# Optimization experiments

Measured on AMD Instinct MI355X. Metric: run time of the kernel, lower is better.

## Reference

```python
import jax, jax.numpy as jnp
import numpy as np

NEG_SLOPE_MLP = 0.1   # F.leaky_relu(x, 0.1) used throughout the repo
NEG_SLOPE_GAT = 0.2   # PyG GATv2Conv default negative_slope
HEADS = 2
OUT = 8


def lrelu(x):
    return jax.nn.leaky_relu(x, NEG_SLOPE_MLP)


def gatv2_conv(x, src, dst, e_attr, wl, bl, wr, br, we, att, bias):
    """PyG-style GATv2Conv with edge features, concat heads.
    x: [N, Din], src/dst: [E], e_attr: [E, 2]
    wl/wr: [heads*out, Din], we: [heads*out, 2], att: [heads, out], bias: [heads*out]
    """
    N = x.shape[0]
    xl = (x @ wl.T + bl).reshape(N, HEADS, OUT)   # source transform
    xr = (x @ wr.T + br).reshape(N, HEADS, OUT)   # target transform
    e = (e_attr @ we.T).reshape(-1, HEADS, OUT)
    m = jax.nn.leaky_relu(xl[src] + xr[dst] + e, NEG_SLOPE_GAT)   # [E, H, O]
    logits = jnp.einsum('ehd,hd->eh', m, att)                      # [E, H]
    # numerically-stable segment softmax over incoming edges of each dst node
    mx = jax.ops.segment_max(logits, dst, num_segments=N)          # [N, H]
    a = jnp.exp(logits - mx[dst])
    denom = jax.ops.segment_sum(a, dst, num_segments=N)
    alpha = a / (denom[dst] + 1e-16)                               # [E, H]
    out = jax.ops.segment_sum(xl[src] * alpha[..., None], dst, num_segments=N)
    return out.reshape(N, HEADS * OUT) + bias                      # [N, 16]


def setup_inputs() -> dict:
    key = jax.random.key(0)
    ks = iter(jax.random.split(key, 64))
    N, E = 250000, 5000000
    inp = {
        'x': jax.random.normal(next(ks), (N, 3), jnp.float32),
        'edge_index': jax.random.randint(next(ks), (2, E), 0, N, jnp.int32),
        'edge_attr': jax.random.normal(next(ks), (E, 2), jnp.float32),
        'meta_data': jax.random.normal(next(ks), (6,), jnp.float32),
    }
    shapes = dict(
        ft1_w=(8, 3), ft1_b=(8,), ft2_w=(8, 8), ft2_b=(8,),
        g1_wl=(16, 8), g1_bl=(16,), g1_wr=(16, 8), g1_br=(16,), g1_we=(16, 2), g1_att=(2, 8), g1_bias=(16,),
        g2_wl=(16, 16), g2_bl=(16,), g2_wr=(16, 16), g2_br=(16,), g2_we=(16, 2), g2_att=(2, 8), g2_bias=(16,),
        sp1_w=(64, 16), sp1_b=(64,), sp2_w=(16, 64), sp2_b=(16,),
        me_w=(8, 6), me_b=(8,),
        fc1_w=(24, 24), fc1_b=(24,), fc2_w=(8, 24), fc2_b=(8,), fc3_w=(3, 8), fc3_b=(3,),
    )
    for name, shp in shapes.items():
        inp[name] = 0.2 * jax.random.normal(next(ks), shp, jnp.float32)
    return inp


def reference(x, edge_index, edge_attr, meta_data,
              ft1_w, ft1_b, ft2_w, ft2_b,
              g1_wl, g1_bl, g1_wr, g1_br, g1_we, g1_att, g1_bias,
              g2_wl, g2_bl, g2_wr, g2_br, g2_we, g2_att, g2_bias,
              sp1_w, sp1_b, sp2_w, sp2_b, me_w, me_b,
              fc1_w, fc1_b, fc2_w, fc2_b, fc3_w, fc3_b):
    src, dst = edge_index[0], edge_index[1]
    # tiny per-node MLP feature transform
    h = lrelu(x @ ft1_w.T + ft1_b)
    h = lrelu(h @ ft2_w.T + ft2_b)                              # [N, 8]
    # 2-layer GATv2 block (activation between layers)
    h = gatv2_conv(h, src, dst, edge_attr, g1_wl, g1_bl, g1_wr, g1_br, g1_we, g1_att, g1_bias)
    h = lrelu(h)
    h = gatv2_conv(h, src, dst, edge_attr, g2_wl, g2_bl, g2_wr, g2_br, g2_we, g2_att, g2_bias)  # [N, 16]
    # sum pool over all nodes + small MLP
    p = h.sum(axis=0)                                           # [16]
    p = lrelu(p @ sp1_w.T + sp1_b)
    p = p @ sp2_w.T + sp2_b                                     # [16]
    # meta data encoder
    m = lrelu(meta_data @ me_w.T + me_b)                        # [8]
    z = jnp.concatenate([p, m], axis=0)                         # [24]
    z = lrelu(z @ fc1_w.T + fc1_b)
    z = lrelu(z @ fc2_w.T + fc2_b)
    # dropout is identity in eval/reference mode
    z = z @ fc3_w.T + fc3_b                                     # [3]
    return jax.nn.softmax(z[None, :], axis=1)                   # [1, 3]
```

## Files before the change

### kernel.cpp

```cpp
#include <hip/hip_runtime.h>
#include <hip/hip_bf16.h>
#include <hip/hip_fp16.h>
#include <math.h>


#define HO 16
#define BSHIFT 8
#define BNODES 256
#define PT 512
#define PCHUNK 6144
#define CAP2 6016

__device__ __forceinline__ float lrelu(float x, float s) { return x > 0.f ? x : s * x; }

__device__ __forceinline__ void store_half8(__half* p, const float* v) {
    __half2 hx[4];
#pragma unroll
    for (int q = 0; q < 4; q++) hx[q] = __floats2half2_rn(v[2*q], v[2*q+1]);
    *reinterpret_cast<uint4*>(p) = *reinterpret_cast<uint4*>(hx);
}

__device__ __forceinline__ void load_half8(const __half* p, float* v) {
    uint4 u = *reinterpret_cast<const uint4*>(p);
    const __half2* h2 = reinterpret_cast<const __half2*>(&u);
#pragma unroll
    for (int q = 0; q < 4; q++) {
        float2 f = __half22float2(h2[q]);
        v[2*q] = f.x; v[2*q+1] = f.y;
    }
}

__global__ void __launch_bounds__(256) node_l1(
    const float* __restrict__ x,
    const float* __restrict__ ft1_w, const float* __restrict__ ft1_b,
    const float* __restrict__ ft2_w, const float* __restrict__ ft2_b,
    const float* __restrict__ wl, const float* __restrict__ bl,
    const float* __restrict__ wr, const float* __restrict__ br,
    __half* __restrict__ xl, float* __restrict__ xr, int N)
{
    int n = blockIdx.x * 256 + threadIdx.x;
    if (n >= N) return;
    float x0 = x[3*n], x1 = x[3*n+1], x2 = x[3*n+2];
    float h1[8];
#pragma unroll
    for (int j = 0; j < 8; j++) {
        float a = ft1_w[3*j]*x0 + ft1_w[3*j+1]*x1 + ft1_w[3*j+2]*x2 + ft1_b[j];
        h1[j] = lrelu(a, 0.1f);
    }
    float h2[8];
#pragma unroll
    for (int j = 0; j < 8; j++) {
        float a = ft2_b[j];
#pragma unroll
        for (int k = 0; k < 8; k++) a += ft2_w[8*j+k]*h1[k];
        h2[j] = lrelu(a, 0.1f);
    }
    float ol[HO], orr[HO];
#pragma unroll
    for (int j = 0; j < HO; j++) {
        float a = bl[j], b = br[j];
#pragma unroll
        for (int k = 0; k < 8; k++) { a += wl[8*j+k]*h2[k]; b += wr[8*j+k]*h2[k]; }
        ol[j] = a; orr[j] = b;
    }
    store_half8(xl + (size_t)n*HO,     ol);
    store_half8(xl + (size_t)n*HO + 8, ol + 8);
    float4* xr4 = (float4*)(xr + (size_t)n*HO);
#pragma unroll
    for (int q = 0; q < 4; q++)
        xr4[q] = make_float4(orr[4*q], orr[4*q+1], orr[4*q+2], orr[4*q+3]);
}

__global__ void __launch_bounds__(256) k_binit(int* __restrict__ bcur)
{
    int b = blockIdx.x * 256 + threadIdx.x;
    if (b < 1024) bcur[b] = b * CAP2;
}

__global__ void __launch_bounds__(PT) k_part(
    const int* __restrict__ src, const int* __restrict__ dst,
    const float* __restrict__ eattr, int* __restrict__ bcur,
    uint2* __restrict__ grecs, int E)
{
    __shared__ int hist[1024], lofs[1024], gofs[1024], lcur[1024];
    __shared__ int scan_s[PT];
    __shared__ uint2 srecs[PCHUNK];
    __shared__ unsigned short bid[PCHUNK];
    int t = threadIdx.x;
    int base = blockIdx.x * PCHUNK;
    int cnt = E - base; if (cnt > PCHUNK) cnt = PCHUNK;

    for (int b = t; b < 1024; b += PT) hist[b] = 0;
    __syncthreads();
    for (int i = t; i < cnt; i += PT)
        atomicAdd(&hist[dst[base + i] >> BSHIFT], 1);
    __syncthreads();
    int h0 = hist[2*t], h1 = hist[2*t+1];
    int pair = h0 + h1;
    scan_s[t] = pair;
    __syncthreads();
    for (int off = 1; off < PT; off <<= 1) {
        int add = (t >= off) ? scan_s[t - off] : 0;
        __syncthreads();
        scan_s[t] += add;
        __syncthreads();
    }
    int pbase = scan_s[t] - pair;
    lofs[2*t]   = pbase;
    lofs[2*t+1] = pbase + h0;
    __syncthreads();
    for (int b = t; b < 1024; b += PT) {
        int c = hist[b];
        int g = (c > 0) ? atomicAdd(&bcur[b], c) : 0;
        gofs[b] = g - lofs[b];
        lcur[b] = 0;
    }
    __syncthreads();
    for (int i = t; i < cnt; i += PT) {
        int e = base + i;
        int d = dst[e];
        int b = d >> BSHIFT;
        float2 ea = ((const float2*)eattr)[e];
        __half2 hv = __floats2half2_rn(ea.x, ea.y);
        unsigned int eb = *reinterpret_cast<unsigned int*>(&hv);
        int q = atomicAdd(&lcur[b], 1);
        int idx = lofs[b] + q;
        srecs[idx] = make_uint2(((unsigned int)src[e] << 8) | (unsigned int)(d & (BNODES-1)), eb);
        bid[idx] = (unsigned short)b;
    }
    __syncthreads();
    for (int i = t; i < cnt; i += PT) {
        int b = bid[i];
        int pos = gofs[b] + i;
        if (pos < (b + 1) * CAP2) grecs[pos] = srecs[i];
    }
}

__global__ void __launch_bounds__(256) k_fine(
    const int* __restrict__ bcur, uint2* recs,
    int* __restrict__ rowS, int* __restrict__ rowE, int N)
{
    __shared__ uint2 rout[CAP2];
    __shared__ int lhist[256], lsc[256], lcur2[256];
    int b = blockIdx.x;
    int bstart = b * CAP2;
    int cnt = bcur[b] - bstart;
    if (cnt > CAP2) cnt = CAP2;
    if (cnt < 0) cnt = 0;
    int t = threadIdx.x;
    lhist[t] = 0;
    __syncthreads();
    for (int i = t; i < cnt; i += 256)
        atomicAdd(&lhist[recs[bstart + i].x & (BNODES-1)], 1);
    __syncthreads();
    int v = lhist[t];
    lsc[t] = v;
    __syncthreads();
    for (int off = 1; off < 256; off <<= 1) {
        int add = (t >= off) ? lsc[t - off] : 0;
        __syncthreads();
        lsc[t] += add;
        __syncthreads();
    }
    int ex = lsc[t] - v;
    lcur2[t] = ex;
    int n = (b << BSHIFT) + t;
    if (n < N) { rowS[n] = bstart + ex; rowE[n] = bstart + ex + v; }
    __syncthreads();
    for (int i = t; i < cnt; i += 256) {
        uint2 r = recs[bstart + i];
        int p = atomicAdd(&lcur2[r.x & (BNODES-1)], 1);
        rout[p] = make_uint2(r.x >> 8, r.y);
    }
    __syncthreads();
    for (int i = t; i < cnt; i += 256)
        recs[bstart + i] = rout[i];
}

struct AggState { float m, s, acc[8]; };

__device__ __forceinline__ void agg_edge(
    AggState& st, const float* va, const float* xd,
    const float* w0, const float* w1, const float* at,
    float ea0, float ea1)
{
    float lg = 0.f;
#pragma unroll
    for (int o = 0; o < 8; o++) {
        float mv = va[o] + xd[o] + (w0[o]*ea0 + w1[o]*ea1);
        mv = mv > 0.f ? mv : 0.2f*mv;
        lg += mv * at[o];
    }
    float nm = fmaxf(st.m, lg);
    float sc = __expf(st.m - nm);
    float wv = __expf(lg - nm);
    st.s = st.s*sc + wv;
#pragma unroll
    for (int o = 0; o < 8; o++) st.acc[o] = st.acc[o]*sc + wv*va[o];
    st.m = nm;
}

__device__ __forceinline__ void agg_node_head(
    int n, int h,
    const int* __restrict__ rowS, const int* __restrict__ rowE,
    const uint2* __restrict__ recs,
    const __half* __restrict__ xl, const float* __restrict__ xr,
    const float* __restrict__ we, const float* __restrict__ att,
    const float* __restrict__ bias, float* out)
{
    int kb = h*8;
    float xd[8], w0[8], w1[8], at[8];
    {
        const float4* xrp = (const float4*)(xr + (size_t)n*HO + kb);
        float4 d0 = xrp[0], d1 = xrp[1];
        xd[0]=d0.x; xd[1]=d0.y; xd[2]=d0.z; xd[3]=d0.w;
        xd[4]=d1.x; xd[5]=d1.y; xd[6]=d1.z; xd[7]=d1.w;
    }
#pragma unroll
    for (int o = 0; o < 8; o++) {
        w0[o] = we[2*(kb+o)];
        w1[o] = we[2*(kb+o)+1];
        at[o] = att[kb+o];
    }
    AggState st;
    st.m = -INFINITY; st.s = 0.f;
#pragma unroll
    for (int o = 0; o < 8; o++) st.acc[o] = 0.f;

    int i = rowS[n], end = rowE[n];
    for (; i + 4 <= end; i += 4) {
        uint2 rA = recs[i], rB = recs[i+1], rC = recs[i+2], rD = recs[i+3];
        float vA[8], vB[8], vC[8], vD[8];
        load_half8(xl + (size_t)rA.x*HO + kb, vA);
        load_half8(xl + (size_t)rB.x*HO + kb, vB);
        load_half8(xl + (size_t)rC.x*HO + kb, vC);
        load_half8(xl + (size_t)rD.x*HO + kb, vD);
        __half2 hA = *reinterpret_cast<__half2*>(&rA.y);
        __half2 hB = *reinterpret_cast<__half2*>(&rB.y);
        __half2 hC = *reinterpret_cast<__half2*>(&rC.y);
        __half2 hD = *reinterpret_cast<__half2*>(&rD.y);
        agg_edge(st, vA, xd, w0, w1, at, __low2float(hA), __high2float(hA));
        agg_edge(st, vB, xd, w0, w1, at, __low2float(hB), __high2float(hB));
        agg_edge(st, vC, xd, w0, w1, at, __low2float(hC), __high2float(hC));
        agg_edge(st, vD, xd, w0, w1, at, __low2float(hD), __high2float(hD));
    }
    for (; i < end; i++) {
        uint2 rA = recs[i];
        float vA[8];
        load_half8(xl + (size_t)rA.x*HO + kb, vA);
        __half2 hA = *reinterpret_cast<__half2*>(&rA.y);
        agg_edge(st, vA, xd, w0, w1, at, __low2float(hA), __high2float(hA));
    }
    float inv = 1.f/(st.s + 1e-16f);
#pragma unroll
    for (int o = 0; o < 8; o++) out[o] = st.acc[o]*inv + bias[kb+o];
}

__global__ void __launch_bounds__(256) node_agg_l1(
    const int* __restrict__ rowS, const int* __restrict__ rowE,
    const uint2* __restrict__ recs,
    const __half* __restrict__ xl, const float* __restrict__ xr,
    const float* __restrict__ we, const float* __restrict__ att,
    const float* __restrict__ bias, float* __restrict__ hout, int N)
{
    int tid = blockIdx.x * 256 + threadIdx.x;
    int n = tid >> 1, h = tid & 1;
    if (n >= N) return;
    float out[8];
    agg_node_head(n, h, rowS, rowE, recs, xl, xr, we, att, bias, out);
    float4* hp = (float4*)(hout + (size_t)n*HO + h*8);
    hp[0] = make_float4(lrelu(out[0],0.1f), lrelu(out[1],0.1f), lrelu(out[2],0.1f), lrelu(out[3],0.1f));
    hp[1] = make_float4(lrelu(out[4],0.1f), lrelu(out[5],0.1f), lrelu(out[6],0.1f), lrelu(out[7],0.1f));
}

__global__ void __launch_bounds__(256) node_transform(
    const float* __restrict__ hin,
    const float* __restrict__ wl2, const float* __restrict__ bl2,
    const float* __restrict__ wr2, const float* __restrict__ br2,
    __half* __restrict__ xl2, float* __restrict__ xr2, int N)
{
    int n = blockIdx.x * 256 + threadIdx.x;
    if (n >= N) return;
    float h[HO];
    const float4* hp = (const float4*)(hin + (size_t)n*HO);
#pragma unroll
    for (int q = 0; q < 4; q++) {
        float4 v = hp[q];
        h[4*q]=v.x; h[4*q+1]=v.y; h[4*q+2]=v.z; h[4*q+3]=v.w;
    }
    float ol[HO], orr[HO];
#pragma unroll
    for (int j = 0; j < HO; j++) {
        float a = bl2[j], b = br2[j];
#pragma unroll
        for (int k = 0; k < HO; k++) { a += wl2[HO*j+k]*h[k]; b += wr2[HO*j+k]*h[k]; }
        ol[j] = a; orr[j] = b;
    }
    store_half8(xl2 + (size_t)n*HO,     ol);
    store_half8(xl2 + (size_t)n*HO + 8, ol + 8);
    float4* xr4 = (float4*)(xr2 + (size_t)n*HO);
#pragma unroll
    for (int q = 0; q < 4; q++)
        xr4[q] = make_float4(orr[4*q], orr[4*q+1], orr[4*q+2], orr[4*q+3]);
}

__global__ void __launch_bounds__(256) node_agg_l2(
    const int* __restrict__ rowS, const int* __restrict__ rowE,
    const uint2* __restrict__ recs,
    const __half* __restrict__ xl, const float* __restrict__ xr,
    const float* __restrict__ we, const float* __restrict__ att,
    const float* __restrict__ bias, float* __restrict__ partials, int pstride, int N)
{
    int tid = blockIdx.x * 256 + threadIdx.x;
    int n = tid >> 1, h = tid & 1;
    float out[8];
    if (n < N) {
        agg_node_head(n, h, rowS, rowE, recs, xl, xr, we, att, bias, out);
    } else {
#pragma unroll
        for (int o = 0; o < 8; o++) out[o] = 0.f;
    }
#pragma unroll
    for (int off = 32; off >= 2; off >>= 1) {
#pragma unroll
        for (int o = 0; o < 8; o++) out[o] += __shfl_down(out[o], off, 64);
    }
    __shared__ float sm[4][2][8];
    int wave = threadIdx.x >> 6, lane = threadIdx.x & 63;
    if (lane < 2) {
#pragma unroll
        for (int o = 0; o < 8; o++) sm[wave][lane][o] = out[o];
    }
    __syncthreads();
    if (threadIdx.x < 16) {
        int hh = threadIdx.x >> 3, oo = threadIdx.x & 7;
        float t = sm[0][hh][oo] + sm[1][hh][oo] + sm[2][hh][oo] + sm[3][hh][oo];
        partials[(size_t)(hh*8 + oo) * pstride + blockIdx.x] = t;
    }
}

__global__ void __launch_bounds__(256) k_reduce(
    const float* __restrict__ partials, int pstride, int nparts,
    float* __restrict__ pool)
{
    __shared__ float s[256];
    int c = blockIdx.x;
    int t = threadIdx.x;
    const float* col = partials + (size_t)c * pstride;
    float acc = 0.f;
    for (int r = t; r < nparts; r += 256) acc += col[r];
    s[t] = acc;
    __syncthreads();
#pragma unroll
    for (int off = 128; off > 0; off >>= 1) {
        if (t < off) s[t] += s[t + off];
        __syncthreads();
    }
    if (t == 0) pool[c] = s[0];
}

__global__ void __launch_bounds__(64) final_mlp(
    const float* __restrict__ pool, const float* __restrict__ meta,
    const float* __restrict__ sp1_w, const float* __restrict__ sp1_b,
    const float* __restrict__ sp2_w, const float* __restrict__ sp2_b,
    const float* __restrict__ me_w, const float* __restrict__ me_b,
    const float* __restrict__ fc1_w, const float* __restrict__ fc1_b,
    const float* __restrict__ fc2_w, const float* __restrict__ fc2_b,
    const float* __restrict__ fc3_w, const float* __restrict__ fc3_b,
    float* __restrict__ out)
{
    __shared__ float s1[64], zb[24], z1[24], z2[8];
    int t = threadIdx.x;
    {
        float acc = sp1_b[t];
        for (int k = 0; k < 16; k++) acc += pool[k]*sp1_w[t*16+k];
        s1[t] = lrelu(acc, 0.1f);
    }
    __syncthreads();
    if (t < 16) {
        float acc = sp2_b[t];
        for (int k = 0; k < 64; k++) acc += s1[k]*sp2_w[t*64+k];
        zb[t] = acc;
    } else if (t < 24) {
        int j = t - 16;
        float acc = me_b[j];
        for (int k = 0; k < 6; k++) acc += meta[k]*me_w[j*6+k];
        zb[t] = lrelu(acc, 0.1f);
    }
    __syncthreads();
    if (t < 24) {
        float acc = fc1_b[t];
        for (int k = 0; k < 24; k++) acc += zb[k]*fc1_w[t*24+k];
        z1[t] = lrelu(acc, 0.1f);
    }
    __syncthreads();
    if (t < 8) {
        float acc = fc2_b[t];
        for (int k = 0; k < 24; k++) acc += z1[k]*fc2_w[t*24+k];
        z2[t] = lrelu(acc, 0.1f);
    }
    __syncthreads();
    if (t == 0) {
        float z3[3]; float mxv = -1e30f;
        for (int j = 0; j < 3; j++) {
            float acc = fc3_b[j];
            for (int k = 0; k < 8; k++) acc += z2[k]*fc3_w[j*8+k];
            z3[j] = acc; mxv = fmaxf(mxv, acc);
        }
        float s = 0.f;
        for (int j = 0; j < 3; j++) { z3[j] = __expf(z3[j]-mxv); s += z3[j]; }
        for (int j = 0; j < 3; j++) out[j] = z3[j]/s;
    }
}

extern "C" void kernel_launch(void* const* d_in, const int* in_sizes, int n_in,
                              void* d_out, int out_size, void* d_ws, size_t ws_size,
                              hipStream_t stream)
{
    const float* x      = (const float*)d_in[0];
    const int*   eidx   = (const int*)  d_in[1];
    const float* eattr  = (const float*)d_in[2];
    const float* meta   = (const float*)d_in[3];
    const float* ft1_w  = (const float*)d_in[4];
    const float* ft1_b  = (const float*)d_in[5];
    const float* ft2_w  = (const float*)d_in[6];
    const float* ft2_b  = (const float*)d_in[7];
    const float* g1_wl  = (const float*)d_in[8];
    const float* g1_bl  = (const float*)d_in[9];
    const float* g1_wr  = (const float*)d_in[10];
    const float* g1_br  = (const float*)d_in[11];
    const float* g1_we  = (const float*)d_in[12];
    const float* g1_att = (const float*)d_in[13];
    const float* g1_bias= (const float*)d_in[14];
    const float* g2_wl  = (const float*)d_in[15];
    const float* g2_bl  = (const float*)d_in[16];
    const float* g2_wr  = (const float*)d_in[17];
    const float* g2_br  = (const float*)d_in[18];
    const float* g2_we  = (const float*)d_in[19];
    const float* g2_att = (const float*)d_in[20];
    const float* g2_bias= (const float*)d_in[21];
    const float* sp1_w  = (const float*)d_in[22];
    const float* sp1_b  = (const float*)d_in[23];
    const float* sp2_w  = (const float*)d_in[24];
    const float* sp2_b  = (const float*)d_in[25];
    const float* me_w   = (const float*)d_in[26];
    const float* me_b   = (const float*)d_in[27];
    const float* fc1_w  = (const float*)d_in[28];
    const float* fc1_b  = (const float*)d_in[29];
    const float* fc2_w  = (const float*)d_in[30];
    const float* fc2_b  = (const float*)d_in[31];
    const float* fc3_w  = (const float*)d_in[32];
    const float* fc3_b  = (const float*)d_in[33];
    float* out = (float*)d_out;

    const int N = in_sizes[0] / 3;
    const int E = in_sizes[2] / 2;
    const int* src = eidx;
    const int* dst = eidx + E;

    const int BN    = (N + 255) / 256;
    const int BN2   = (2*N + 255) / 256;
    const int NBUCK = (N + BNODES - 1) >> BSHIFT;
    const int BP    = (E + PCHUNK - 1) / PCHUNK;
    const int pstride = (BN2 + 63) & ~63;

    char* w = (char*)d_ws;
    size_t off = 0;
    auto take = [&](size_t bytes) { size_t o = off; off += (bytes + 255) & ~(size_t)255; return o; };
    int*    rowS     = (int*)   (w + take((size_t)4*N));
    int*    rowE     = (int*)   (w + take((size_t)4*N));
    int*    bcur     = (int*)   (w + take(4096));
    float*  pool     = (float*) (w + take(64));
    float*  partials = (float*) (w + take((size_t)4*16*pstride));
    uint2*  recs     = (uint2*) (w + take((size_t)8*NBUCK*CAP2));
    __half* xl       = (__half*)(w + take((size_t)32*N));
    float*  xr       = (float*) (w + take((size_t)64*N));
    float*  hbuf     = (float*) (w + take((size_t)64*N));

    node_l1<<<BN, 256, 0, stream>>>(x, ft1_w, ft1_b, ft2_w, ft2_b,
                                    g1_wl, g1_bl, g1_wr, g1_br, xl, xr, N);
    k_binit<<<4, 256, 0, stream>>>(bcur);
    k_part<<<BP, PT, 0, stream>>>(src, dst, eattr, bcur, recs, E);
    k_fine<<<NBUCK, 256, 0, stream>>>(bcur, recs, rowS, rowE, N);

    node_agg_l1<<<BN2, 256, 0, stream>>>(rowS, rowE, recs, xl, xr,
                                         g1_we, g1_att, g1_bias, hbuf, N);
    node_transform<<<BN, 256, 0, stream>>>(hbuf, g2_wl, g2_bl, g2_wr, g2_br, xl, xr, N);
    node_agg_l2<<<BN2, 256, 0, stream>>>(rowS, rowE, recs, xl, xr,
                                         g2_we, g2_att, g2_bias, partials, pstride, N);
    k_reduce<<<16, 256, 0, stream>>>(partials, pstride, BN2, pool);
    final_mlp<<<1, 64, 0, stream>>>(pool, meta, sp1_w, sp1_b, sp2_w, sp2_b,
                                    me_w, me_b, fc1_w, fc1_b, fc2_w, fc2_b,
                                    fc3_w, fc3_b, out);
}
```

Measured before the change: 468.8 us.

## Store source features in FP8 and fuse layer-2 transform into layer-1 aggregation

Source-transformed node features (xl) are now packed as 8-bit FP8 with the hardware pack/unpack builtins instead of FP16, halving the bytes fetched per gathered edge in both aggregation kernels. The separate node_transform kernel and the fp32 hidden buffer are removed: layer-1 aggregation swaps head halves between thread pairs via shuffle and computes the layer-2 xl/xr directly. Using separate xlA/xlB buffers avoids a read/write race, but xr is overwritten in place, which stays safe only because each thread reads its own xr slice before writing it. FP8 quantisation noticeably reduces precision of the features used in the logits and outputs, so accuracy may degrade.

New measurement: 420.9 us. 1.11x faster.

```diff
diff --git a/kernel.cpp b/kernel.cpp
--- a/kernel.cpp
+++ b/kernel.cpp
@@ -11,23 +11,25 @@
 #define PCHUNK 6144
 #define CAP2 6016
 
+typedef __attribute__((ext_vector_type(2))) float v2f;
+
 __device__ __forceinline__ float lrelu(float x, float s) { return x > 0.f ? x : s * x; }
 
-__device__ __forceinline__ void store_half8(__half* p, const float* v) {
-    __half2 hx[4];
-#pragma unroll
-    for (int q = 0; q < 4; q++) hx[q] = __floats2half2_rn(v[2*q], v[2*q+1]);
-    *reinterpret_cast<uint4*>(p) = *reinterpret_cast<uint4*>(hx);
-}
-
-__device__ __forceinline__ void load_half8(const __half* p, float* v) {
-    uint4 u = *reinterpret_cast<const uint4*>(p);
-    const __half2* h2 = reinterpret_cast<const __half2*>(&u);
-#pragma unroll
-    for (int q = 0; q < 4; q++) {
-        float2 f = __half22float2(h2[q]);
-        v[2*q] = f.x; v[2*q+1] = f.y;
-    }
+__device__ __forceinline__ uint2 pack_fp8x8(const float* v) {
+    int a = __builtin_amdgcn_cvt_pk_fp8_f32(v[0], v[1], 0, false);
+    a     = __builtin_amdgcn_cvt_pk_fp8_f32(v[2], v[3], a, true);
+    int b = __builtin_amdgcn_cvt_pk_fp8_f32(v[4], v[5], 0, false);
+    b     = __builtin_amdgcn_cvt_pk_fp8_f32(v[6], v[7], b, true);
+    return make_uint2((unsigned int)a, (unsigned int)b);
+}
+
+__device__ __forceinline__ void unpack_fp8x8(uint2 u, float* v) {
+    v2f f0 = __builtin_amdgcn_cvt_pk_f32_fp8((int)u.x, false);
+    v2f f1 = __builtin_amdgcn_cvt_pk_f32_fp8((int)u.x, true);
+    v2f f2 = __builtin_amdgcn_cvt_pk_f32_fp8((int)u.y, false);
+    v2f f3 = __builtin_amdgcn_cvt_pk_f32_fp8((int)u.y, true);
+    v[0]=f0.x; v[1]=f0.y; v[2]=f1.x; v[3]=f1.y;
+    v[4]=f2.x; v[5]=f2.y; v[6]=f3.x; v[7]=f3.y;
 }
 
 __global__ void __launch_bounds__(256) node_l1(
@@ -36,7 +38,7 @@
     const float* __restrict__ ft2_w, const float* __restrict__ ft2_b,
     const float* __restrict__ wl, const float* __restrict__ bl,
     const float* __restrict__ wr, const float* __restrict__ br,
-    __half* __restrict__ xl, float* __restrict__ xr, int N)
+    uint2* __restrict__ xlA, float* __restrict__ xr, int N)
 {
     int n = blockIdx.x * 256 + threadIdx.x;
     if (n >= N) return;
@@ -63,8 +65,9 @@
         for (int k = 0; k < 8; k++) { a += wl[8*j+k]*h2[k]; b += wr[8*j+k]*h2[k]; }
         ol[j] = a; orr[j] = b;
     }
-    store_half8(xl + (size_t)n*HO,     ol);
-    store_half8(xl + (size_t)n*HO + 8, ol + 8);
+    uint2 p0 = pack_fp8x8(ol);
+    uint2 p1 = pack_fp8x8(ol + 8);
+    ((uint4*)xlA)[n] = make_uint4(p0.x, p0.y, p1.x, p1.y);
     float4* xr4 = (float4*)(xr + (size_t)n*HO);
 #pragma unroll
     for (int q = 0; q < 4; q++)
@@ -204,7 +207,7 @@
     int n, int h,
     const int* __restrict__ rowS, const int* __restrict__ rowE,
     const uint2* __restrict__ recs,
-    const __half* __restrict__ xl, const float* __restrict__ xr,
+    const uint2* __restrict__ xl8, const float* __restrict__ xr,
     const float* __restrict__ we, const float* __restrict__ att,
     const float* __restrict__ bias, float* out)
 {
@@ -230,11 +233,13 @@
     int i = rowS[n], end = rowE[n];
     for (; i + 4 <= end; i += 4) {
         uint2 rA = recs[i], rB = recs[i+1], rC = recs[i+2], rD = recs[i+3];
+        uint2 gA = xl8[(size_t)rA.x*2 + h];
+        uint2 gB = xl8[(size_t)rB.x*2 + h];
+        uint2 gC = xl8[(size_t)rC.x*2 + h];
+        uint2 gD = xl8[(size_t)rD.x*2 + h];
         float vA[8], vB[8], vC[8], vD[8];
-        load_half8(xl + (size_t)rA.x*HO + kb, vA);
-        load_half8(xl + (size_t)rB.x*HO + kb, vB);
-        load_half8(xl + (size_t)rC.x*HO + kb, vC);
-        load_half8(xl + (size_t)rD.x*HO + kb, vD);
+        unpack_fp8x8(gA, vA); unpack_fp8x8(gB, vB);
+        unpack_fp8x8(gC, vC); unpack_fp8x8(gD, vD);
         __half2 hA = *reinterpret_cast<__half2*>(&rA.y);
         __half2 hB = *reinterpret_cast<__half2*>(&rB.y);
         __half2 hC = *reinterpret_cast<__half2*>(&rC.y);
@@ -246,8 +251,9 @@
     }
     for (; i < end; i++) {
         uint2 rA = recs[i];
+        uint2 gA = xl8[(size_t)rA.x*2 + h];
         float vA[8];
-        load_half8(xl + (size_t)rA.x*HO + kb, vA);
+        unpack_fp8x8(gA, vA);
         __half2 hA = *reinterpret_cast<__half2*>(&rA.y);
         agg_edge(st, vA, xd, w0, w1, at, __low2float(hA), __high2float(hA));
     }
@@ -259,55 +265,48 @@
 __global__ void __launch_bounds__(256) node_agg_l1(
     const int* __restrict__ rowS, const int* __restrict__ rowE,
     const uint2* __restrict__ recs,
-    const __half* __restrict__ xl, const float* __restrict__ xr,
+    const uint2* __restrict__ xlA, float* xr,
     const float* __restrict__ we, const float* __restrict__ att,
-    const float* __restrict__ bias, float* __restrict__ hout, int N)
+    const float* __restrict__ bias,
+    const float* __restrict__ wl2, const float* __restrict__ bl2,
+    const float* __restrict__ wr2, const float* __restrict__ br2,
+    uint2* __restrict__ xlB, int N)
 {
     int tid = blockIdx.x * 256 + threadIdx.x;
     int n = tid >> 1, h = tid & 1;
     if (n >= N) return;
+    int kb = h*8;
     float out[8];
-    agg_node_head(n, h, rowS, rowE, recs, xl, xr, we, att, bias, out);
-    float4* hp = (float4*)(hout + (size_t)n*HO + h*8);
-    hp[0] = make_float4(lrelu(out[0],0.1f), lrelu(out[1],0.1f), lrelu(out[2],0.1f), lrelu(out[3],0.1f));
-    hp[1] = make_float4(lrelu(out[4],0.1f), lrelu(out[5],0.1f), lrelu(out[6],0.1f), lrelu(out[7],0.1f));
-}
-
-__global__ void __launch_bounds__(256) node_transform(
-    const float* __restrict__ hin,
-    const float* __restrict__ wl2, const float* __restrict__ bl2,
-    const float* __restrict__ wr2, const float* __restrict__ br2,
-    __half* __restrict__ xl2, float* __restrict__ xr2, int N)
-{
-    int n = blockIdx.x * 256 + threadIdx.x;
-    if (n >= N) return;
-    float h[HO];
-    const float4* hp = (const float4*)(hin + (size_t)n*HO);
-#pragma unroll
-    for (int q = 0; q < 4; q++) {
-        float4 v = hp[q];
-        h[4*q]=v.x; h[4*q+1]=v.y; h[4*q+2]=v.z; h[4*q+3]=v.w;
-    }
-    float ol[HO], orr[HO];
-#pragma unroll
-    for (int j = 0; j < HO; j++) {
+    agg_node_head(n, h, rowS, rowE, recs, xlA, xr, we, att, bias, out);
+    float hh[8];
+#pragma unroll
+    for (int o = 0; o < 8; o++) hh[o] = lrelu(out[o], 0.1f);
+    float hfull[HO];
+#pragma unroll
+    for (int o = 0; o < 8; o++) {
+        float hp = __shfl_xor(hh[o], 1, 64);
+        hfull[kb + o] = hh[o];
+        hfull[(kb ^ 8) + o] = hp;
+    }
+    float ol[8], orr[8];
+#pragma unroll
+    for (int jo = 0; jo < 8; jo++) {
+        int j = kb + jo;
         float a = bl2[j], b = br2[j];
 #pragma unroll
-        for (int k = 0; k < HO; k++) { a += wl2[HO*j+k]*h[k]; b += wr2[HO*j+k]*h[k]; }
-        ol[j] = a; orr[j] = b;
-    }
-    store_half8(xl2 + (size_t)n*HO,     ol);
-    store_half8(xl2 + (size_t)n*HO + 8, ol + 8);
-    float4* xr4 = (float4*)(xr2 + (size_t)n*HO);
-#pragma unroll
-    for (int q = 0; q < 4; q++)
-        xr4[q] = make_float4(orr[4*q], orr[4*q+1], orr[4*q+2], orr[4*q+3]);
+        for (int k = 0; k < HO; k++) { a += wl2[HO*j+k]*hfull[k]; b += wr2[HO*j+k]*hfull[k]; }
+        ol[jo] = a; orr[jo] = b;
+    }
+    xlB[(size_t)n*2 + h] = pack_fp8x8(ol);
+    float4* xr4 = (float4*)(xr + (size_t)n*HO + kb);
+    xr4[0] = make_float4(orr[0], orr[1], orr[2], orr[3]);
+    xr4[1] = make_float4(orr[4], orr[5], orr[6], orr[7]);
 }
 
 __global__ void __launch_bounds__(256) node_agg_l2(
     const int* __restrict__ rowS, const int* __restrict__ rowE,
     const uint2* __restrict__ recs,
-    const __half* __restrict__ xl, const float* __restrict__ xr,
+    const uint2* __restrict__ xlB, const float* __restrict__ xr,
     const float* __restrict__ we, const float* __restrict__ att,
     const float* __restrict__ bias, float* __restrict__ partials, int pstride, int N)
 {
@@ -315,7 +314,7 @@
     int n = tid >> 1, h = tid & 1;
     float out[8];
     if (n < N) {
-        agg_node_head(n, h, rowS, rowE, recs, xl, xr, we, att, bias, out);
+        agg_node_head(n, h, rowS, rowE, recs, xlB, xr, we, att, bias, out);
     } else {
 #pragma unroll
         for (int o = 0; o < 8; o++) out[o] = 0.f;
@@ -473,20 +472,20 @@
     float*  pool     = (float*) (w + take(64));
     float*  partials = (float*) (w + take((size_t)4*16*pstride));
     uint2*  recs     = (uint2*) (w + take((size_t)8*NBUCK*CAP2));
-    __half* xl       = (__half*)(w + take((size_t)32*N));
+    uint2*  xlA      = (uint2*) (w + take((size_t)16*N));
+    uint2*  xlB      = (uint2*) (w + take((size_t)16*N));
     float*  xr       = (float*) (w + take((size_t)64*N));
-    float*  hbuf     = (float*) (w + take((size_t)64*N));
 
     node_l1<<<BN, 256, 0, stream>>>(x, ft1_w, ft1_b, ft2_w, ft2_b,
-                                    g1_wl, g1_bl, g1_wr, g1_br, xl, xr, N);
+                                    g1_wl, g1_bl, g1_wr, g1_br, xlA, xr, N);
     k_binit<<<4, 256, 0, stream>>>(bcur);
     k_part<<<BP, PT, 0, stream>>>(src, dst, eattr, bcur, recs, E);
     k_fine<<<NBUCK, 256, 0, stream>>>(bcur, recs, rowS, rowE, N);
 
-    node_agg_l1<<<BN2, 256, 0, stream>>>(rowS, rowE, recs, xl, xr,
-                                         g1_we, g1_att, g1_bias, hbuf, N);
-    node_transform<<<BN, 256, 0, stream>>>(hbuf, g2_wl, g2_bl, g2_wr, g2_br, xl, xr, N);
-    node_agg_l2<<<BN2, 256, 0, stream>>>(rowS, rowE, recs, xl, xr,
+    node_agg_l1<<<BN2, 256, 0, stream>>>(rowS, rowE, recs, xlA, xr,
+                                         g1_we, g1_att, g1_bias,
+                                         g2_wl, g2_bl, g2_wr, g2_br, xlB, N);
+    node_agg_l2<<<BN2, 256, 0, stream>>>(rowS, rowE, recs, xlB, xr,
                                          g2_we, g2_att, g2_bias, partials, pstride, N);
     k_reduce<<<16, 256, 0, stream>>>(partials, pstride, BN2, pool);
     final_mlp<<<1, 64, 0, stream>>>(pool, meta, sp1_w, sp1_b, sp2_w, sp2_b,
```
